# Optimization experiments

Hardware: AMD Instinct MI355X
Metric: run time of the kernel (lower is better)

The kernel has to match this reference:

```python
import jax, jax.numpy as jnp
import numpy as np

K_NODES = 512  # per-expert capacity (k_nodes init arg)


def setup_inputs() -> dict:
    key = jax.random.key(0)
    k1, k2, k3, k4 = jax.random.split(key, 4)
    B_T, D, E = 16384, 512, 64
    x = jax.random.normal(k1, (B_T, D, 2), jnp.float32)
    # gate: orthogonal_(gain=0.1) ~ small-scale dense matrix
    gate_weights = jax.random.normal(k2, (2 * D, E), jnp.float32) * (0.1 / np.sqrt(2 * D))
    # ComplexKaimingInitializer: |N(0,1)|/sqrt(fan_in) magnitude, uniform phase
    mag = jnp.abs(jax.random.normal(k3, (E, D, D), jnp.float32)) / np.sqrt(D)
    phase = jax.random.uniform(k4, (E, D, D), jnp.float32, minval=0.0, maxval=2.0 * np.pi)
    experts_w = jnp.stack([mag * jnp.cos(phase), mag * jnp.sin(phase)], axis=-1)  # [E,D,D,2]
    act_bias = jnp.zeros((D,), jnp.float32)
    return {"x": x, "gate_weights": gate_weights, "experts_w": experts_w, "act_bias": act_bias}


def reference(x, gate_weights, experts_w, act_bias):
    # x: [B_T, D, 2] interleaved-real tokens
    B_T, D, _ = x.shape
    E = gate_weights.shape[1]
    k = min(B_T, K_NODES)

    # --- expert-choice routing: each expert picks its top-k tokens ---
    scores = jnp.nan_to_num(x.reshape(B_T, 2 * D) @ gate_weights)  # [B_T, E]
    topk_scores, topk_idx = jax.lax.top_k(scores.T, k)             # [E, k] each

    # --- gather tokens per expert (row-major [E, k] order, as in forward()) ---
    flat_gather = topk_idx.reshape(-1)                  # [E*k]
    xb = x[flat_gather].reshape(E, k, D, 2)             # [E, k, D, 2]
    xr, xi = xb[..., 0], xb[..., 1]
    wr, wi = experts_w[..., 0], experts_w[..., 1]

    # --- grouped complex GEMM as 4 real batched matmuls ---
    yr = jnp.einsum('ekd,edf->ekf', xr, wr) - jnp.einsum('ekd,edf->ekf', xi, wi)
    yi = jnp.einsum('ekd,edf->ekf', xr, wi) + jnp.einsum('ekd,edf->ekf', xi, wr)
    y = jnp.nan_to_num(jnp.stack([yr, yi], axis=-1))    # [E, k, D, 2]

    # weight by routing scores, then scatter-add combine
    y_weighted = (y * topk_scores[..., None, None]).reshape(E * k, D, 2)
    # NOTE: original code scatters with topk_indices.T.reshape(-1) (column-major
    # w.r.t. the [E,k] gather order). Reproduced faithfully.
    flat_scatter = topk_idx.T.reshape(-1)               # [E*k]
    out = jnp.zeros((B_T, D, 2), jnp.float32).at[flat_scatter].add(y_weighted)
    counts = jnp.zeros((B_T,), jnp.float32).at[flat_scatter].add(1.0)
    agg = out / jnp.maximum(counts, 1.0)[:, None, None]

    # ComplexGELU: exact (erf) GELU on real/imag parts with shared bias
    res = jax.nn.gelu(agg + act_bias[:, None], approximate=False)  # [B_T, D, 2]
    return res
```

## Files before the change

### kernel.cpp

```cpp
#include <hip/hip_runtime.h>
#include <stdint.h>
#include <math.h>

typedef uint32_t u32;
typedef uint64_t u64;
typedef unsigned short u16;

#define B_T    16384
#define DD     512
#define NE     64
#define KCAP   512
#define TWO_D  1024

typedef __attribute__((ext_vector_type(8))) short bf16x8;
typedef __attribute__((ext_vector_type(4))) float f32x4;
typedef __attribute__((ext_vector_type(4))) u32 u32x4;

static __device__ __forceinline__ u32 mono_of(float s) {
  u32 b = __float_as_uint(s);
  return (b & 0x80000000u) ? ~b : (b | 0x80000000u);
}
static __device__ __forceinline__ float score_from_mono(u32 m) {
  u32 b = (m & 0x80000000u) ? (m ^ 0x80000000u) : ~m;
  return __uint_as_float(b);
}
static __device__ __forceinline__ u16 f2bf(float f) {
  u32 b = __float_as_uint(f);
  b += 0x7FFFu + ((b >> 16) & 1u);
  return (u16)(b >> 16);
}
static __device__ __forceinline__ u32 f2bf2(float lo, float hi) {
  return (u32)f2bf(lo) | ((u32)f2bf(hi) << 16);
}
static __device__ __forceinline__ float bf2f(u32 u) {
  return __uint_as_float(u << 16);
}
static __device__ __forceinline__ u32 cvtpk(float lo, float hi) {
  u32 r;
  asm("v_cvt_pk_bf16_f32 %0, %1, %2" : "=v"(r) : "v"(lo), "v"(hi));
  return r;
}
static __device__ __forceinline__ void gload_lds16(const u16* g, u16* l) {
  __builtin_amdgcn_global_load_lds(
      (const __attribute__((address_space(1))) u32*)(g),
      (__attribute__((address_space(3))) u32*)(l), 16, 0, 0);
}
static __device__ __forceinline__ bf16x8 negbf8(bf16x8 v) {
  u32x4 u;
  u32x4 s = *reinterpret_cast<u32x4*>(&v);
  u[0] = s[0] ^ 0x80008000u;
  u[1] = s[1] ^ 0x80008000u;
  u[2] = s[2] ^ 0x80008000u;
  u[3] = s[3] ^ 0x80008000u;
  return *reinterpret_cast<bf16x8*>(&u);
}

__global__ __launch_bounds__(256) void k0_xconv(const float* __restrict__ x,
                                                u16* __restrict__ xrb,
                                                u16* __restrict__ xib) {
  int idx = blockIdx.x * 256 + threadIdx.x;
  float4 v = reinterpret_cast<const float4*>(x)[idx];
  reinterpret_cast<u32*>(xrb)[idx] = f2bf2(v.x, v.z);
  reinterpret_cast<u32*>(xib)[idx] = f2bf2(v.y, v.w);
}

__global__ __launch_bounds__(256) void k1_gate(const float* __restrict__ x,
                                               const float* __restrict__ gw,
                                               float* __restrict__ scoresT) {
  __shared__ __align__(16) float xs[128][32];
  __shared__ __align__(16) float gs[128][64];
  const int tb  = blockIdx.x * 32;
  const int tid = threadIdx.x;
  const int tx = tid & 7, ty = tid >> 3;

  float accC[2][4];
  float accT[2][4];
#pragma unroll
  for (int i = 0; i < 2; ++i)
#pragma unroll
    for (int j = 0; j < 4; ++j) { accC[i][j] = 0.f; accT[i][j] = 0.f; }

  for (int c = 0; c < 8; ++c) {
    const int k0 = c * 128;
    {
      const int t = tid & 31, ks = (tid >> 5) * 16;
      const float* src = x + (size_t)(tb + t) * TWO_D + k0 + ks;
#pragma unroll
      for (int i = 0; i < 4; ++i) {
        float4 v = reinterpret_cast<const float4*>(src)[i];
        xs[ks + i * 4 + 0][t] = v.x;
        xs[ks + i * 4 + 1][t] = v.y;
        xs[ks + i * 4 + 2][t] = v.z;
        xs[ks + i * 4 + 3][t] = v.w;
      }
      const float4* gsrc = reinterpret_cast<const float4*>(gw + (size_t)k0 * 64);
      float4* gdst = reinterpret_cast<float4*>(&gs[0][0]);
#pragma unroll
      for (int i = 0; i < 8; ++i) gdst[tid + i * 256] = gsrc[tid + i * 256];
    }
    __syncthreads();
    for (int k = 0; k < 128; ++k) {
      float4 a4 = *reinterpret_cast<float4*>(&xs[k][tx * 4]);
      float2 b2 = *reinterpret_cast<float2*>(&gs[k][ty * 2]);
      float av[4] = {a4.x, a4.y, a4.z, a4.w};
      float bv[2] = {b2.x, b2.y};
#pragma unroll
      for (int i = 0; i < 2; ++i)
#pragma unroll
        for (int j = 0; j < 4; ++j) accC[i][j] = fmaf(bv[i], av[j], accC[i][j]);
    }
    __syncthreads();
    if (c == 3 || c == 7) {
#pragma unroll
      for (int i = 0; i < 2; ++i)
#pragma unroll
        for (int j = 0; j < 4; ++j) {
          accT[i][j] = accT[i][j] + accC[i][j];
          accC[i][j] = 0.f;
        }
    }
  }
#pragma unroll
  for (int i = 0; i < 2; ++i) {
    float4 v = make_float4(accT[i][0], accT[i][1], accT[i][2], accT[i][3]);
    *reinterpret_cast<float4*>(&scoresT[(size_t)(ty * 2 + i) * B_T + tb + tx * 4]) = v;
  }
}

__global__ __launch_bounds__(1024) void k2_topk(const float* __restrict__ scoresT,
                                                int* __restrict__ topk_idx,
                                                float* __restrict__ topk_scr,
                                                int* __restrict__ counts,
                                                int* __restrict__ entries) {
  const int e = blockIdx.x, tid = threadIdx.x;
  const float* row = scoresT + (size_t)e * B_T;
  __shared__ u32 keys[B_T];
  __shared__ u32 hist[256];
  __shared__ u32 s_prefix, s_r;
  __shared__ u32 cnt_gt, cnt_eq;
  __shared__ u64 skey[512];
  __shared__ u32 tie[512];

#pragma unroll
  for (int i = 0; i < 4; ++i) {
    int v4 = i * 1024 + tid;
    float4 v = reinterpret_cast<const float4*>(row)[v4];
    keys[v4 * 4 + 0] = mono_of(v.x);
    keys[v4 * 4 + 1] = mono_of(v.y);
    keys[v4 * 4 + 2] = mono_of(v.z);
    keys[v4 * 4 + 3] = mono_of(v.w);
  }
  if (tid == 0) { s_prefix = 0; s_r = KCAP; cnt_gt = 0; cnt_eq = 0; }
  u32 prefmask = 0;
  __syncthreads();

  for (int pass = 0; pass < 4; ++pass) {
    const int shift = 24 - 8 * pass;
    if (tid < 256) hist[tid] = 0;
    __syncthreads();
    const u32 prefix = s_prefix;
    for (int t = tid; t < B_T; t += 1024) {
      u32 m = keys[t];
      if ((m & prefmask) == prefix) atomicAdd(&hist[(m >> shift) & 0xFFu], 1u);
    }
    __syncthreads();
    if (tid == 0) {
      u32 r = s_r, cum = 0;
      int sel = 0;
      for (int b = 255; b >= 0; --b) {
        if (cum + hist[b] >= r) { sel = b; s_r = r - cum; break; }
        cum += hist[b];
      }
      s_prefix = prefix | ((u32)sel << shift);
    }
    prefmask |= (0xFFu << shift);
    __syncthreads();
  }

  const u32 kmono = s_prefix;
  const u32 rneed = s_r;

  for (int t = tid; t < B_T; t += 1024) {
    u32 m = keys[t];
    if (m > kmono) {
      u32 p = atomicAdd(&cnt_gt, 1u);
      if (p < 512) skey[p] = ((u64)(~m) << 32) | (u32)t;
    } else if (m == kmono) {
      u32 p = atomicAdd(&cnt_eq, 1u);
      if (p < 512) tie[p] = (u32)t;
    }
  }
  __syncthreads();

  const u32 ngt = cnt_gt;
  const u32 ne = cnt_eq < 512u ? cnt_eq : 512u;
  if (tid < ne) {
    u32 my = tie[tid];
    u32 rank = 0;
    for (u32 j = 0; j < ne; ++j) rank += (tie[j] < my) ? 1u : 0u;
    if (rank < rneed) skey[ngt + rank] = ((u64)(~kmono) << 32) | my;
  }
  __syncthreads();

  if (tid < 512) {
    u64 my = skey[tid];
    u32 rank = 0;
    for (int j = 0; j < 512; ++j) rank += (skey[j] < my) ? 1u : 0u;
    u32 idx = (u32)my;
    u32 m = ~((u32)(my >> 32));
    topk_idx[e * KCAP + rank] = (int)idx;
    topk_scr[e * KCAP + rank] = score_from_mono(m);
    int pos = atomicAdd(&counts[idx], 1);
    entries[idx * 64 + pos] = (int)(rank * 64 + e);
  }
}

__global__ __launch_bounds__(256) void k3_wtrans(const float* __restrict__ w,
                                                 u16* __restrict__ wrT,
                                                 u16* __restrict__ wiT) {
  __shared__ float2 tr[32][33];
  const int bid = blockIdx.x;
  const int e = bid >> 8, tile = bid & 255;
  const int d0 = (tile >> 4) * 32, f0 = (tile & 15) * 32;
  const int tid = threadIdx.x;
  const int fl2 = tid & 15, dl0 = tid >> 4;
  const float* base = w + ((size_t)e * 512 + d0) * 1024 + (size_t)f0 * 2;
#pragma unroll
  for (int it = 0; it < 2; ++it) {
    int dl = dl0 + it * 16;
    float4 v = *reinterpret_cast<const float4*>(base + (size_t)dl * 1024 + fl2 * 4);
    tr[dl][fl2 * 2]     = make_float2(v.x, v.y);
    tr[dl][fl2 * 2 + 1] = make_float2(v.z, v.w);
  }
  __syncthreads();
  const int d2 = (tid & 15) * 2, fl0 = tid >> 4;
#pragma unroll
  for (int it = 0; it < 2; ++it) {
    int f = fl0 + it * 16;
    float2 a = tr[d2][f], b = tr[d2 + 1][f];
    size_t off = ((size_t)e * 512 + f0 + f) * 512 + d0 + d2;
    *reinterpret_cast<u32*>(&wrT[off]) = f2bf2(a.x, b.x);
    *reinterpret_cast<u32*>(&wiT[off]) = f2bf2(a.y, b.y);
  }
}

__global__ __launch_bounds__(256, 2) void k4_pre(
    const u16* __restrict__ xrb, const u16* __restrict__ xib,
    const int* __restrict__ topk_idx, const float* __restrict__ topk_scr,
    const u16* __restrict__ wrT, const u16* __restrict__ wiT,
    u16* __restrict__ yrw, u16* __restrict__ yiw) {
  const int bid = blockIdx.x;
  const int xcd = bid & 7, q = bid >> 3, t = q & 15, g = q >> 4;
  const int e = g * 8 + xcd;
  const int mb = t & 3, fb = t >> 2;
  const int m0 = mb * 128, f0 = fb * 128;

  __shared__ __align__(16) u16 Ar[2][4096];
  __shared__ __align__(16) u16 Ai[2][4096];
  __shared__ __align__(16) u16 Bu[2][4096];
  __shared__ __align__(16) u16 Bv[2][4096];
  __shared__ int tok[128];
  __shared__ float scr[128];

  const int tid = threadIdx.x;
  if (tid < 128) {
    tok[tid] = topk_idx[e * KCAP + m0 + tid];
    scr[tid] = topk_scr[e * KCAP + m0 + tid];
  }
  __syncthreads();

  const int r0  = tid & 127;
  const int ka0 = (tid >> 7) * 8;
  const int ka1 = ka0 + 16;
  const size_t brow = ((size_t)e * 512 + f0 + r0) * 512;
  const size_t arow = (size_t)tok[r0] * 512;
  const int wv = tid >> 6, ln = tid & 63;
  const int d0 = wv * 512;
  const int d1 = 2048 + wv * 512;

  const int mbase = (wv >> 1) * 64, nbase = (wv & 1) * 64;
  const int frow = ln & 15, fq = ln >> 4;
  const int ra = fq * 1024 + (mbase + frow) * 8;
  const int rb = fq * 1024 + (nbase + frow) * 8;

  f32x4 accR[4][4] = {};
  f32x4 accI[4][4] = {};

#define STAGE(b, kk)                                         \
  do {                                                       \
    gload_lds16(wrT + brow + (kk) + ka0, Bu[b] + d0);        \
    gload_lds16(wrT + brow + (kk) + ka1, Bu[b] + d1);        \
    gload_lds16(wiT + brow + (kk) + ka0, Bv[b] + d0);        \
    gload_lds16(wiT + brow + (kk) + ka1, Bv[b] + d1);        \
    gload_lds16(xrb + arow + (kk) + ka0, Ar[b] + d0);        \
    gload_lds16(xrb + arow + (kk) + ka1, Ar[b] + d1);        \
    gload_lds16(xib + arow + (kk) + ka0, Ai[b] + d0);        \
    gload_lds16(xib + arow + (kk) + ka1, Ai[b] + d1);        \
  } while (0)

  STAGE(0, 0);
  __syncthreads();

  for (int s = 0; s < 16; ++s) {
    const int b = s & 1;
    if (s < 15) STAGE(b ^ 1, (s + 1) * 32);

    bf16x8 ar[4], ai[4], bu[4], bv[4];
#pragma unroll
    for (int m = 0; m < 4; ++m) {
      ar[m] = *reinterpret_cast<const bf16x8*>(&Ar[b][ra + m * 128]);
      ai[m] = *reinterpret_cast<const bf16x8*>(&Ai[b][ra + m * 128]);
    }
#pragma unroll
    for (int n = 0; n < 4; ++n) {
      bu[n] = *reinterpret_cast<const bf16x8*>(&Bu[b][rb + n * 128]);
      bv[n] = *reinterpret_cast<const bf16x8*>(&Bv[b][rb + n * 128]);
    }
#pragma unroll
    for (int m = 0; m < 4; ++m)
#pragma unroll
      for (int n = 0; n < 4; ++n) {
        bf16x8 bw = negbf8(bv[n]);
        accR[m][n] = __builtin_amdgcn_mfma_f32_16x16x32_bf16(ar[m], bu[n], accR[m][n], 0, 0, 0);
        accR[m][n] = __builtin_amdgcn_mfma_f32_16x16x32_bf16(ai[m], bw,    accR[m][n], 0, 0, 0);
        accI[m][n] = __builtin_amdgcn_mfma_f32_16x16x32_bf16(ar[m], bv[n], accI[m][n], 0, 0, 0);
        accI[m][n] = __builtin_amdgcn_mfma_f32_16x16x32_bf16(ai[m], bu[n], accI[m][n], 0, 0, 0);
      }
    __syncthreads();
  }
#undef STAGE

  const int rr = fq * 4;
#pragma unroll
  for (int m = 0; m < 4; ++m) {
#pragma unroll
    for (int r = 0; r < 4; ++r) {
      const int jl = mbase + m * 16 + rr + r;
      const float ww = scr[jl];
      const size_t ybase = ((size_t)e * KCAP + m0 + jl) * DD;
#pragma unroll
      for (int n = 0; n < 4; ++n) {
        const int fg = f0 + nbase + n * 16 + frow;
        yrw[ybase + fg] = f2bf(accR[m][n][r] * ww);
        yiw[ybase + fg] = f2bf(accI[m][n][r] * ww);
      }
    }
  }
}

__global__ __launch_bounds__(256, 2) void k4_fb(
    const float* __restrict__ x, const int* __restrict__ topk_idx,
    const float* __restrict__ topk_scr, const u16* __restrict__ wrT,
    const u16* __restrict__ wiT, u16* __restrict__ yrw, u16* __restrict__ yiw) {
  const int bid = blockIdx.x;
  const int xcd = bid & 7, q = bid >> 3, t = q & 15, g = q >> 4;
  const int e = g * 8 + xcd;
  const int mb = t & 3, fb = t >> 2;
  const int m0 = mb * 128, f0 = fb * 128;

  __shared__ __align__(16) u16 Ar[4096];
  __shared__ __align__(16) u16 Ai[4096];
  __shared__ __align__(16) u16 Bu[4096];
  __shared__ __align__(16) u16 Bv[4096];
  __shared__ int tok[128];
  __shared__ float scr[128];

  const int tid = threadIdx.x;
  if (tid < 128) {
    tok[tid] = topk_idx[e * KCAP + m0 + tid];
    scr[tid] = topk_scr[e * KCAP + m0 + tid];
  }
  __syncthreads();

  const int r0  = tid & 127;
  const int ka0 = (tid >> 7) * 8;
  const int ka1 = ka0 + 16;
  const size_t brow = ((size_t)e * 512 + f0 + r0) * 512;
  const int wv = tid >> 6, ln = tid & 63;
  const int d0 = wv * 512;
  const int d1 = 2048 + wv * 512;

  const int row = tid >> 1, half = tid & 1;
  const float* arow_f = x + (size_t)tok[row] * TWO_D + half * 32;

  const int mbase = (wv >> 1) * 64, nbase = (wv & 1) * 64;
  const int frow = ln & 15, fq = ln >> 4;
  const int ra = fq * 1024 + (mbase + frow) * 8;
  const int rb = fq * 1024 + (nbase + frow) * 8;

  f32x4 accR[4][4] = {};
  f32x4 accI[4][4] = {};

  for (int step = 0; step < 16; ++step) {
    const int k0 = step * 32;
    gload_lds16(wrT + brow + k0 + ka0, Bu + d0);
    gload_lds16(wrT + brow + k0 + ka1, Bu + d1);
    gload_lds16(wiT + brow + k0 + ka0, Bv + d0);
    gload_lds16(wiT + brow + k0 + ka1, Bv + d1);
    {
      const float4* ap = reinterpret_cast<const float4*>(arow_f + (size_t)k0 * 2);
      u32 xr[8], xi[8];
#pragma unroll
      for (int i = 0; i < 8; ++i) {
        float4 v = ap[i];
        xr[i] = cvtpk(v.x, v.z);
        xi[i] = cvtpk(v.y, v.w);
      }
      uint4 wa, wb;
      wa.x = xr[0]; wa.y = xr[1]; wa.z = xr[2]; wa.w = xr[3];
      wb.x = xr[4]; wb.y = xr[5]; wb.z = xr[6]; wb.w = xr[7];
      *reinterpret_cast<uint4*>(&Ar[(2 * half) * 1024 + row * 8]) = wa;
      *reinterpret_cast<uint4*>(&Ar[(2 * half + 1) * 1024 + row * 8]) = wb;
      wa.x = xi[0]; wa.y = xi[1]; wa.z = xi[2]; wa.w = xi[3];
      wb.x = xi[4]; wb.y = xi[5]; wb.z = xi[6]; wb.w = xi[7];
      *reinterpret_cast<uint4*>(&Ai[(2 * half) * 1024 + row * 8]) = wa;
      *reinterpret_cast<uint4*>(&Ai[(2 * half + 1) * 1024 + row * 8]) = wb;
    }
    __syncthreads();

    bf16x8 ar[4], ai[4], bu[4], bv[4];
#pragma unroll
    for (int m = 0; m < 4; ++m) {
      ar[m] = *reinterpret_cast<const bf16x8*>(&Ar[ra + m * 128]);
      ai[m] = *reinterpret_cast<const bf16x8*>(&Ai[ra + m * 128]);
    }
#pragma unroll
    for (int n = 0; n < 4; ++n) {
      bu[n] = *reinterpret_cast<const bf16x8*>(&Bu[rb + n * 128]);
      bv[n] = *reinterpret_cast<const bf16x8*>(&Bv[rb + n * 128]);
    }
#pragma unroll
    for (int m = 0; m < 4; ++m)
#pragma unroll
      for (int n = 0; n < 4; ++n) {
        bf16x8 bw = negbf8(bv[n]);
        accR[m][n] = __builtin_amdgcn_mfma_f32_16x16x32_bf16(ar[m], bu[n], accR[m][n], 0, 0, 0);
        accR[m][n] = __builtin_amdgcn_mfma_f32_16x16x32_bf16(ai[m], bw,    accR[m][n], 0, 0, 0);
        accI[m][n] = __builtin_amdgcn_mfma_f32_16x16x32_bf16(ar[m], bv[n], accI[m][n], 0, 0, 0);
        accI[m][n] = __builtin_amdgcn_mfma_f32_16x16x32_bf16(ai[m], bu[n], accI[m][n], 0, 0, 0);
      }
    __syncthreads();
  }

  const int rr = fq * 4;
#pragma unroll
  for (int m = 0; m < 4; ++m) {
#pragma unroll
    for (int r = 0; r < 4; ++r) {
      const int jl = mbase + m * 16 + rr + r;
      const float ww = scr[jl];
      const size_t ybase = ((size_t)e * KCAP + m0 + jl) * DD;
#pragma unroll
      for (int n = 0; n < 4; ++n) {
        const int fg = f0 + nbase + n * 16 + frow;
        yrw[ybase + fg] = f2bf(accR[m][n][r] * ww);
        yiw[ybase + fg] = f2bf(accI[m][n][r] * ww);
      }
    }
  }
}

#define GELU(z) (0.5f * (z) * (1.0f + erff((z)*0.70710678118654752440f)))
__global__ __launch_bounds__(256) void k5_gather(
    const u16* __restrict__ yrw, const u16* __restrict__ yiw,
    const int* __restrict__ counts, const int* __restrict__ entries,
    const float* __restrict__ bias, float* __restrict__ out) {
  const int t = blockIdx.x;
  const int tid = threadIdx.x;
  const int c = counts[t];
  const float inv = 1.0f / (float)(c > 0 ? c : 1);
  const int f0 = tid * 2;
  float sr0 = 0.f, sr1 = 0.f, si0 = 0.f, si1 = 0.f;
  for (int i = 0; i < c; ++i) {
    int srcrow = entries[t * 64 + i];
    size_t off = (size_t)srcrow * DD + f0;
    u32 pr = *reinterpret_cast<const u32*>(yrw + off);
    u32 pi = *reinterpret_cast<const u32*>(yiw + off);
    sr0 += bf2f(pr & 0xFFFFu); sr1 += bf2f(pr >> 16);
    si0 += bf2f(pi & 0xFFFFu); si1 += bf2f(pi >> 16);
  }
  const float b0 = bias[f0], b1 = bias[f0 + 1];
  float v0 = sr0 * inv + b0;
  float v1 = si0 * inv + b0;
  float v2 = sr1 * inv + b1;
  float v3 = si1 * inv + b1;
  float4 o = make_float4(GELU(v0), GELU(v1), GELU(v2), GELU(v3));
  *reinterpret_cast<float4*>(&out[(size_t)t * TWO_D + f0 * 2]) = o;
}

extern "C" void kernel_launch(void* const* d_in, const int* in_sizes, int n_in,
                              void* d_out, int out_size, void* d_ws, size_t ws_size,
                              hipStream_t stream) {
  const float* x    = (const float*)d_in[0];
  const float* gw   = (const float*)d_in[1];
  const float* w    = (const float*)d_in[2];
  const float* bias = (const float*)d_in[3];
  float* out = (float*)d_out;

  char* ws = (char*)d_ws;
  u16*   yrw     = (u16*)(ws);
  float* scoresT = (float*)(ws);
  u16*   yiw     = (u16*)(ws + 33554432);
  int*   tidx    = (int*)(ws + 67108864);
  float* tscr    = (float*)(ws + 67239936);
  int*   counts  = (int*)(ws + 67371008);
  int*   entries = (int*)(ws + 67436544);
  u16*   wrT     = (u16*)(ws + 71630848);
  u16*   wiT     = (u16*)(ws + 105185280);
  u16*   xrb     = (u16*)(ws + 138739712);
  u16*   xib     = (u16*)(ws + 155516928);

  const bool preconv = ws_size >= 172294144ull;

  hipMemsetAsync(counts, 0, B_T * sizeof(int), stream);
  k1_gate<<<B_T / 32, 256, 0, stream>>>(x, gw, scoresT);
  k2_topk<<<NE, 1024, 0, stream>>>(scoresT, tidx, tscr, counts, entries);
  k3_wtrans<<<NE * 256, 256, 0, stream>>>(w, wrT, wiT);
  if (preconv) {
    k0_xconv<<<16384, 256, 0, stream>>>(x, xrb, xib);
    k4_pre<<<1024, 256, 0, stream>>>(xrb, xib, tidx, tscr, wrT, wiT, yrw, yiw);
  } else {
    k4_fb<<<1024, 256, 0, stream>>>(x, tidx, tscr, wrT, wiT, yrw, yiw);
  }
  k5_gather<<<B_T, 256, 0, stream>>>(yrw, yiw, counts, entries, bias, out);
}
```

Measured before the change: 290.7 us.

## Fuse x bf16 conversion into gate kernel and deepen GEMM LDS prefetch

Removes the separate x-to-bf16 conversion kernel by writing split real/imag bf16 copies of x from the gate kernel while it already streams x, which saves a full re-read of x and one launch. The grouped complex GEMM now issues two stages of global-to-LDS loads up front and uses explicit vmcnt waits with raw barriers, so one stage can be in flight while the other is computed. This relies on hand-counted vmcnt values, and in the fallback path the gate kernel writes scratch bf16 data into the yiw region, which is then overwritten.

```diff
diff --git a/kernel.cpp b/kernel.cpp
--- a/kernel.cpp
+++ b/kernel.cpp
@@ -55,18 +55,11 @@
   return *reinterpret_cast<bf16x8*>(&u);
 }
 
-__global__ __launch_bounds__(256) void k0_xconv(const float* __restrict__ x,
-                                                u16* __restrict__ xrb,
-                                                u16* __restrict__ xib) {
-  int idx = blockIdx.x * 256 + threadIdx.x;
-  float4 v = reinterpret_cast<const float4*>(x)[idx];
-  reinterpret_cast<u32*>(xrb)[idx] = f2bf2(v.x, v.z);
-  reinterpret_cast<u32*>(xib)[idx] = f2bf2(v.y, v.w);
-}
-
 __global__ __launch_bounds__(256) void k1_gate(const float* __restrict__ x,
                                                const float* __restrict__ gw,
-                                               float* __restrict__ scoresT) {
+                                               float* __restrict__ scoresT,
+                                               u16* __restrict__ xrb,
+                                               u16* __restrict__ xib) {
   __shared__ __align__(16) float xs[128][32];
   __shared__ __align__(16) float gs[128][64];
   const int tb  = blockIdx.x * 32;
@@ -85,6 +78,7 @@
     {
       const int t = tid & 31, ks = (tid >> 5) * 16;
       const float* src = x + (size_t)(tb + t) * TWO_D + k0 + ks;
+      u32 rr[4], ii[4];
 #pragma unroll
       for (int i = 0; i < 4; ++i) {
         float4 v = reinterpret_cast<const float4*>(src)[i];
@@ -92,7 +86,16 @@
         xs[ks + i * 4 + 1][t] = v.y;
         xs[ks + i * 4 + 2][t] = v.z;
         xs[ks + i * 4 + 3][t] = v.w;
+        rr[i] = f2bf2(v.x, v.z);
+        ii[i] = f2bf2(v.y, v.w);
       }
+      const size_t xoff = (size_t)(tb + t) * 512 + c * 64 + (ks >> 1);
+      uint4 wr, wi;
+      wr.x = rr[0]; wr.y = rr[1]; wr.z = rr[2]; wr.w = rr[3];
+      wi.x = ii[0]; wi.y = ii[1]; wi.z = ii[2]; wi.w = ii[3];
+      *reinterpret_cast<uint4*>(xrb + xoff) = wr;
+      *reinterpret_cast<uint4*>(xib + xoff) = wi;
+
       const float4* gsrc = reinterpret_cast<const float4*>(gw + (size_t)k0 * 64);
       float4* gdst = reinterpret_cast<float4*>(&gs[0][0]);
 #pragma unroll
@@ -298,37 +301,43 @@
     gload_lds16(xib + arow + (kk) + ka1, Ai[b] + d1);        \
   } while (0)
 
+#define COMPUTE(b)                                                                              \
+  do {                                                                                          \
+    bf16x8 ar[4], ai[4], bu[4], bv[4];                                                          \
+    _Pragma("unroll") for (int m = 0; m < 4; ++m) {                                             \
+      ar[m] = *reinterpret_cast<const bf16x8*>(&Ar[b][ra + m * 128]);                           \
+      ai[m] = *reinterpret_cast<const bf16x8*>(&Ai[b][ra + m * 128]);                           \
+    }                                                                                           \
+    _Pragma("unroll") for (int n = 0; n < 4; ++n) {                                             \
+      bu[n] = *reinterpret_cast<const bf16x8*>(&Bu[b][rb + n * 128]);                           \
+      bv[n] = *reinterpret_cast<const bf16x8*>(&Bv[b][rb + n * 128]);                           \
+    }                                                                                           \
+    _Pragma("unroll") for (int m = 0; m < 4; ++m)                                               \
+      _Pragma("unroll") for (int n = 0; n < 4; ++n) {                                           \
+        bf16x8 bw = negbf8(bv[n]);                                                              \
+        accR[m][n] = __builtin_amdgcn_mfma_f32_16x16x32_bf16(ar[m], bu[n], accR[m][n], 0, 0, 0);\
+        accR[m][n] = __builtin_amdgcn_mfma_f32_16x16x32_bf16(ai[m], bw,    accR[m][n], 0, 0, 0);\
+        accI[m][n] = __builtin_amdgcn_mfma_f32_16x16x32_bf16(ar[m], bv[n], accI[m][n], 0, 0, 0);\
+        accI[m][n] = __builtin_amdgcn_mfma_f32_16x16x32_bf16(ai[m], bu[n], accI[m][n], 0, 0, 0);\
+      }                                                                                         \
+  } while (0)
+
   STAGE(0, 0);
-  __syncthreads();
-
-  for (int s = 0; s < 16; ++s) {
+  STAGE(1, 32);
+
+  for (int s = 0; s < 15; ++s) {
     const int b = s & 1;
-    if (s < 15) STAGE(b ^ 1, (s + 1) * 32);
-
-    bf16x8 ar[4], ai[4], bu[4], bv[4];
-#pragma unroll
-    for (int m = 0; m < 4; ++m) {
-      ar[m] = *reinterpret_cast<const bf16x8*>(&Ar[b][ra + m * 128]);
-      ai[m] = *reinterpret_cast<const bf16x8*>(&Ai[b][ra + m * 128]);
-    }
-#pragma unroll
-    for (int n = 0; n < 4; ++n) {
-      bu[n] = *reinterpret_cast<const bf16x8*>(&Bu[b][rb + n * 128]);
-      bv[n] = *reinterpret_cast<const bf16x8*>(&Bv[b][rb + n * 128]);
-    }
-#pragma unroll
-    for (int m = 0; m < 4; ++m)
-#pragma unroll
-      for (int n = 0; n < 4; ++n) {
-        bf16x8 bw = negbf8(bv[n]);
-        accR[m][n] = __builtin_amdgcn_mfma_f32_16x16x32_bf16(ar[m], bu[n], accR[m][n], 0, 0, 0);
-        accR[m][n] = __builtin_amdgcn_mfma_f32_16x16x32_bf16(ai[m], bw,    accR[m][n], 0, 0, 0);
-        accI[m][n] = __builtin_amdgcn_mfma_f32_16x16x32_bf16(ar[m], bv[n], accI[m][n], 0, 0, 0);
-        accI[m][n] = __builtin_amdgcn_mfma_f32_16x16x32_bf16(ai[m], bu[n], accI[m][n], 0, 0, 0);
-      }
-    __syncthreads();
-  }
+    asm volatile("s_waitcnt vmcnt(8)" ::: "memory");
+    __builtin_amdgcn_s_barrier();
+    COMPUTE(b);
+    __builtin_amdgcn_s_barrier();
+    if (s + 2 < 16) STAGE(b, (s + 2) * 32);
+  }
+  asm volatile("s_waitcnt vmcnt(0)" ::: "memory");
+  __builtin_amdgcn_s_barrier();
+  COMPUTE(1);
 #undef STAGE
+#undef COMPUTE
 
   const int rr = fq * 4;
 #pragma unroll
@@ -513,13 +522,16 @@
   const bool preconv = ws_size >= 172294144ull;
 
   hipMemsetAsync(counts, 0, B_T * sizeof(int), stream);
-  k1_gate<<<B_T / 32, 256, 0, stream>>>(x, gw, scoresT);
-  k2_topk<<<NE, 1024, 0, stream>>>(scoresT, tidx, tscr, counts, entries);
-  k3_wtrans<<<NE * 256, 256, 0, stream>>>(w, wrT, wiT);
   if (preconv) {
-    k0_xconv<<<16384, 256, 0, stream>>>(x, xrb, xib);
+    k1_gate<<<B_T / 32, 256, 0, stream>>>(x, gw, scoresT, xrb, xib);
+    k2_topk<<<NE, 1024, 0, stream>>>(scoresT, tidx, tscr, counts, entries);
+    k3_wtrans<<<NE * 256, 256, 0, stream>>>(w, wrT, wiT);
     k4_pre<<<1024, 256, 0, stream>>>(xrb, xib, tidx, tscr, wrT, wiT, yrw, yiw);
   } else {
+    k1_gate<<<B_T / 32, 256, 0, stream>>>(x, gw, scoresT, (u16*)(ws + 33554432),
+                                          (u16*)(ws + 33554432 + 16777216));
+    k2_topk<<<NE, 1024, 0, stream>>>(scoresT, tidx, tscr, counts, entries);
+    k3_wtrans<<<NE * 256, 256, 0, stream>>>(w, wrT, wiT);
     k4_fb<<<1024, 256, 0, stream>>>(x, tidx, tscr, wrT, wiT, yrw, yiw);
   }
   k5_gather<<<B_T, 256, 0, stream>>>(yrw, yiw, counts, entries, bias, out);
```

Result: faster. 272.4 us (-6.3%).
